# Kernel optimization log

Hardware: AMD Instinct MI355X
Metric: run time of the kernel (lower is better)

Reference implementation:

```python
import jax, jax.numpy as jnp
import numpy as np

V = 20000
E = 40000
NODE_IN = 74
EDGE_IN = 12
D = 64            # node_out_feats
EH = 128          # edge_hidden_feats
STEPS = 6         # num_step_message_passing


def setup_inputs() -> dict:
    key = jax.random.key(0)
    ks = jax.random.split(key, 16)
    s = lambda k, shape, scale=0.05: jax.random.normal(k, shape, dtype=jnp.float32) * scale
    return {
        "node_feats": jax.random.normal(ks[0], (V, NODE_IN), dtype=jnp.float32),
        "edge_feats": jax.random.normal(ks[1], (E, EDGE_IN), dtype=jnp.float32),
        "src": jax.random.randint(ks[2], (E,), 0, V),
        "dst": jax.random.randint(ks[3], (E,), 0, V),
        # project_node_feats: Linear(NODE_IN, D) + ReLU
        "proj_W": s(ks[4], (D, NODE_IN)),
        "proj_b": jnp.zeros((D,), jnp.float32),
        # NNConv edge network: Linear(EDGE_IN, EH) -> ReLU -> Linear(EH, D*D)
        "en_W1": s(ks[5], (EH, EDGE_IN)),
        "en_b1": jnp.zeros((EH,), jnp.float32),
        "en_W2": s(ks[6], (D * D, EH)),
        "en_b2": jnp.zeros((D * D,), jnp.float32),
        # NNConv output bias
        "conv_b": jnp.zeros((D,), jnp.float32),
        # single-layer GRU (PyTorch gate order r, z, n)
        "gru_Wih": s(ks[7], (3 * D, D)),
        "gru_Whh": s(ks[8], (3 * D, D)),
        "gru_bih": jnp.zeros((3 * D,), jnp.float32),
        "gru_bhh": jnp.zeros((3 * D,), jnp.float32),
        # MLPPredictor: Linear(2*D, 1)
        "pred_W": s(ks[9], (1, 2 * D)),
        "pred_b": jnp.zeros((1,), jnp.float32),
    }


def reference(node_feats, edge_feats, src, dst, proj_W, proj_b,
              en_W1, en_b1, en_W2, en_b2, conv_b,
              gru_Wih, gru_Whh, gru_bih, gru_bhh, pred_W, pred_b):
    nV = node_feats.shape[0]
    # project node features
    h = jax.nn.relu(node_feats @ proj_W.T + proj_b)  # (V, D)
    # per-edge weight matrices from the edge network (constant across steps)
    ew = jax.nn.relu(edge_feats @ en_W1.T + en_b1) @ en_W2.T + en_b2  # (E, D*D)
    ew = ew.reshape(-1, D, D)  # (E, D, D)

    def step(h, _):
        # NNConv (aggregator='sum'): m_e = h[src_e] @ W_e, sum at dst, + bias
        m = jnp.einsum('ei,eio->eo', h[src], ew)               # (E, D)
        neigh = jax.ops.segment_sum(m, dst, num_segments=nV)   # (V, D)
        x = jax.nn.relu(neigh + conv_b)
        # GRU update; hidden == h (they coincide in the original loop)
        gi = x @ gru_Wih.T + gru_bih
        gh = h @ gru_Whh.T + gru_bhh
        i_r, i_z, i_n = jnp.split(gi, 3, axis=-1)
        h_r, h_z, h_n = jnp.split(gh, 3, axis=-1)
        r = jax.nn.sigmoid(i_r + h_r)
        z = jax.nn.sigmoid(i_z + h_z)
        n = jnp.tanh(i_n + r * h_n)
        h_new = (1.0 - z) * n + z * h
        return h_new, None

    h, _ = jax.lax.scan(step, h, None, length=STEPS)
    # MLPPredictor: per-edge gather-concat-linear
    score = jnp.concatenate([h[src], h[dst]], axis=1) @ pred_W.T + pred_b  # (E, 1)
    return score
```

## Files before the change

### kernel.cpp

```cpp
#include <hip/hip_runtime.h>
#include <hip/hip_bf16.h>
#include <cstdint>

#define NV 20000
#define NE 40000
#define NODE_IN 74
#define EDGE_IN 12
#define D 64
#define EHID 128
#define NSTEPS 6

typedef __bf16 bf16x8 __attribute__((ext_vector_type(8)));
typedef float f32x4 __attribute__((ext_vector_type(4)));

__global__ __launch_bounds__(256) void k_proj(const float* __restrict__ nf,
                                              const float* __restrict__ W,
                                              const float* __restrict__ b,
                                              float* __restrict__ h,
                                              float* __restrict__ neigh) {
  __shared__ float sn[4][NODE_IN];
  int tid = threadIdx.x;
  int nb = blockIdx.x * 4;
  for (int idx = tid; idx < 4 * NODE_IN; idx += 256) {
    int r = idx / NODE_IN, c = idx % NODE_IN;
    sn[r][c] = nf[(size_t)(nb + r) * NODE_IN + c];
  }
  __syncthreads();
  int nl = tid >> 6, o = tid & 63;
  float acc = b[o];
#pragma unroll
  for (int i = 0; i < NODE_IN; ++i) acc = fmaf(sn[nl][i], W[o * NODE_IN + i], acc);
  h[(size_t)(nb + nl) * D + o] = fmaxf(acc, 0.f);
  neigh[(size_t)(nb + nl) * D + o] = 0.f;
}

__global__ __launch_bounds__(256) void k_edge1(const float* __restrict__ ef,
                                               const float* __restrict__ W1,
                                               const float* __restrict__ b1,
                                               __hip_bfloat16* __restrict__ t_bf) {
  __shared__ float se[2][EDGE_IN];
  int tid = threadIdx.x;
  int eb = blockIdx.x * 2;
  if (tid < 2 * EDGE_IN)
    se[tid / EDGE_IN][tid % EDGE_IN] =
        ef[(size_t)(eb + tid / EDGE_IN) * EDGE_IN + tid % EDGE_IN];
  __syncthreads();
  int el = tid >> 7, k = tid & 127;
  float acc = b1[k];
#pragma unroll
  for (int j = 0; j < EDGE_IN; ++j) acc = fmaf(se[el][j], W1[k * EDGE_IN + j], acc);
  t_bf[(size_t)(eb + el) * EHID + k] = __float2bfloat16(fmaxf(acc, 0.f));
}

__global__ __launch_bounds__(256) void k_cvt_w2(const float* __restrict__ W2,
                                                __hip_bfloat16* __restrict__ w2b) {
  int idx = blockIdx.x * 256 + threadIdx.x;
  if (idx < D * D * EHID) w2b[idx] = __float2bfloat16(W2[idx]);
}

__global__ __launch_bounds__(256) void k_b2t(const float* __restrict__ b2,
                                             __hip_bfloat16* __restrict__ b2t) {
  int idx = blockIdx.x * 256 + threadIdx.x;
  int o = idx >> 6, i = idx & 63;
  b2t[o * 64 + i] = __float2bfloat16(b2[i * 64 + o]);
}

__global__ __launch_bounds__(256) void k_build_b(const float* __restrict__ Wih,
                                                 const float* __restrict__ Whh,
                                                 __hip_bfloat16* __restrict__ Bhi,
                                                 __hip_bfloat16* __restrict__ Blo) {
  int idx = blockIdx.x * 256 + threadIdx.x;
  int n = idx >> 7, k = idx & 127;
  int o = n & 63, cls = n >> 6;
  float v;
  if (cls == 0)      v = (k < 64) ? Wih[o * 64 + k]         : Whh[o * 64 + (k - 64)];
  else if (cls == 1) v = (k < 64) ? Wih[(64 + o) * 64 + k]  : Whh[(64 + o) * 64 + (k - 64)];
  else if (cls == 2) v = (k < 64) ? Wih[(128 + o) * 64 + k] : 0.f;
  else               v = (k < 64) ? 0.f                     : Whh[(128 + o) * 64 + (k - 64)];
  __hip_bfloat16 hi = __float2bfloat16(v);
  Bhi[idx] = hi;
  Blo[idx] = __float2bfloat16(v - __bfloat162float(hi));
}

__global__ __launch_bounds__(512, 2) void k_msg(const float* __restrict__ h,
                                                const __hip_bfloat16* __restrict__ t_bf,
                                                const __hip_bfloat16* __restrict__ w2,
                                                const __hip_bfloat16* __restrict__ b2t,
                                                const int* __restrict__ src,
                                                const int* __restrict__ dst,
                                                float* __restrict__ neigh) {
  __shared__ __hip_bfloat16 W2s[512 * 128];
  __shared__ __hip_bfloat16 Hs[8][16 * 64];
  int tid = threadIdx.x;
  int bx = blockIdx.x;
  int cg = bx >> 6, ih = (bx >> 5) & 1, s = bx & 31;
  int lane = tid & 63, lr = lane & 15, lq = lane >> 4;
  int wave = tid >> 6;
  const int ocol = cg * 16 + lr;

#pragma unroll
  for (int it = 0; it < 16; ++it) {
    int chunk = it * 512 + tid;
    int row = chunk >> 4, c = chunk & 15;
    int ig = row >> 4, ol = row & 15;
    const __hip_bfloat16* gp =
        w2 + ((size_t)((ih * 32 + ig) * 64 + cg * 16 + ol)) * EHID + c * 8;
    *(bf16x8*)(W2s + row * 128 + ((c ^ ol) * 8)) = *(const bf16x8*)gp;
  }
  bf16x8 b2f0, b2f1;
#pragma unroll
  for (int j = 0; j < 8; ++j) {
    int k = lq * 8 + j;
    __bf16 v = *(const __bf16*)(b2t + (size_t)ocol * 64 + ih * 32 + k);
    __bf16 z = (__bf16)0.0f;
    b2f0[j] = (k < 16) ? v : z;
    b2f1[j] = (k >= 16) ? v : z;
  }
  __syncthreads();

  __hip_bfloat16* Hsw = &Hs[wave][0];
  int e0s = s * 1280;
  int nt = (s < 31) ? 20 : 5;

  int sw0 = (((0 * 4 + lq) ^ lr) * 8);
  int sw1 = (((1 * 4 + lq) ^ lr) * 8);
  int sw2 = (((2 * 4 + lq) ^ lr) * 8);
  int sw3 = (((3 * 4 + lq) ^ lr) * 8);

#pragma unroll 1
  for (int r3 = 0; r3 < 3; ++r3) {
    int t = r3 * 8 + wave;
    if (t >= nt) break;
    int e0t = e0s + t * 64;

    bf16x8 tf[4][4];
#pragma unroll
    for (int mt = 0; mt < 4; ++mt)
#pragma unroll
      for (int ks = 0; ks < 4; ++ks)
        tf[mt][ks] = *(const bf16x8*)(t_bf + (size_t)(e0t + mt * 16 + lr) * EHID +
                                      ks * 32 + lq * 8);

    int s_e = src[e0t + lane];
    const float* hrow = h + (size_t)s_e * D + ih * 32;
    f32x4 C[4];
#pragma unroll
    for (int mt = 0; mt < 4; ++mt) C[mt] = f32x4{0.f, 0.f, 0.f, 0.f};

#pragma unroll
    for (int ph = 0; ph < 2; ++ph) {
#pragma unroll
      for (int q = 0; q < 4; ++q) {
        float4 hv = *(const float4*)(hrow + ph * 16 + q * 4);
        Hsw[(q * 4 + 0) * 64 + lane] = __float2bfloat16(hv.x);
        Hsw[(q * 4 + 1) * 64 + lane] = __float2bfloat16(hv.y);
        Hsw[(q * 4 + 2) * 64 + lane] = __float2bfloat16(hv.z);
        Hsw[(q * 4 + 3) * 64 + lane] = __float2bfloat16(hv.w);
      }
#pragma unroll
      for (int mt = 0; mt < 4; ++mt) {
        bf16x8 af;
#pragma unroll
        for (int j = 0; j < 8; ++j)
          af[j] = *(const __bf16*)(Hsw + ((lq * 8 + j) & 15) * 64 + mt * 16 + lr);
        C[mt] = __builtin_amdgcn_mfma_f32_16x16x32_bf16(af, ph ? b2f1 : b2f0, C[mt], 0, 0, 0);
      }
#pragma unroll 2
      for (int igl = 0; igl < 16; ++igl) {
        int ig = ph * 16 + igl;
        const __hip_bfloat16* Wr = W2s + (ig * 16 + lr) * 128;
        bf16x8 f0 = *(const bf16x8*)(Wr + sw0);
        bf16x8 f1 = *(const bf16x8*)(Wr + sw1);
        bf16x8 f2 = *(const bf16x8*)(Wr + sw2);
        bf16x8 f3 = *(const bf16x8*)(Wr + sw3);
#pragma unroll
        for (int mt = 0; mt < 4; ++mt) {
          f32x4 P = {0.f, 0.f, 0.f, 0.f};
          P = __builtin_amdgcn_mfma_f32_16x16x32_bf16(tf[mt][0], f0, P, 0, 0, 0);
          P = __builtin_amdgcn_mfma_f32_16x16x32_bf16(tf[mt][1], f1, P, 0, 0, 0);
          P = __builtin_amdgcn_mfma_f32_16x16x32_bf16(tf[mt][2], f2, P, 0, 0, 0);
          P = __builtin_amdgcn_mfma_f32_16x16x32_bf16(tf[mt][3], f3, P, 0, 0, 0);
          uint2 hA = *(const uint2*)(Hsw + igl * 64 + mt * 16 + lq * 4);
          C[mt][0] = fmaf(__uint_as_float(hA.x << 16), P[0], C[mt][0]);
          C[mt][1] = fmaf(__uint_as_float(hA.x & 0xffff0000u), P[1], C[mt][1]);
          C[mt][2] = fmaf(__uint_as_float(hA.y << 16), P[2], C[mt][2]);
          C[mt][3] = fmaf(__uint_as_float(hA.y & 0xffff0000u), P[3], C[mt][3]);
        }
      }
    }
#pragma unroll
    for (int mt = 0; mt < 4; ++mt) {
#pragma unroll
      for (int r = 0; r < 4; ++r) {
        int ea = e0t + mt * 16 + lq * 4 + r;
        atomicAdd(neigh + (size_t)dst[ea] * D + ocol, C[mt][r]);
      }
    }
  }
}

__global__ __launch_bounds__(256) void k_gru(float* __restrict__ neigh,
                                             float* __restrict__ h,
                                             const __hip_bfloat16* __restrict__ Bhi,
                                             const __hip_bfloat16* __restrict__ Blo,
                                             const float* __restrict__ cb,
                                             const float* __restrict__ bih,
                                             const float* __restrict__ bhh) {
  __shared__ __hip_bfloat16 Ahi[32 * 128];
  __shared__ __hip_bfloat16 Alo[32 * 128];
  int tid = threadIdx.x;
  int n0 = blockIdx.x * 32;
  for (int idx = tid; idx < 32 * 64; idx += 256) {
    int node = idx >> 6, f = idx & 63;
    int gn = n0 + node;
    float xv = fmaxf(neigh[(size_t)gn * D + f] + cb[f], 0.f);
    neigh[(size_t)gn * D + f] = 0.f;
    float hv = h[(size_t)gn * D + f];
    __hip_bfloat16 xh = __float2bfloat16(xv);
    __hip_bfloat16 hh = __float2bfloat16(hv);
    Ahi[node * 128 + f] = xh;
    Ahi[node * 128 + 64 + f] = hh;
    Alo[node * 128 + f] = __float2bfloat16(xv - __bfloat162float(xh));
    Alo[node * 128 + 64 + f] = __float2bfloat16(hv - __bfloat162float(hh));
  }
  __syncthreads();
  int wave = tid >> 6, lane = tid & 63;
  int lr = lane & 15, lq = lane >> 4;
  f32x4 acc[2][4] = {};
#pragma unroll
  for (int ks = 0; ks < 4; ++ks) {
    int koff = ks * 32 + lq * 8;
    bf16x8 ah[2], al[2], bh[4], bl[4];
#pragma unroll
    for (int mt = 0; mt < 2; ++mt) {
      ah[mt] = *(const bf16x8*)(Ahi + (mt * 16 + lr) * 128 + koff);
      al[mt] = *(const bf16x8*)(Alo + (mt * 16 + lr) * 128 + koff);
    }
#pragma unroll
    for (int cls = 0; cls < 4; ++cls) {
      int n = cls * 64 + wave * 16 + lr;
      bh[cls] = *(const bf16x8*)(Bhi + (size_t)n * 128 + koff);
      bl[cls] = *(const bf16x8*)(Blo + (size_t)n * 128 + koff);
    }
#pragma unroll
    for (int mt = 0; mt < 2; ++mt)
#pragma unroll
      for (int cls = 0; cls < 4; ++cls) {
        acc[mt][cls] = __builtin_amdgcn_mfma_f32_16x16x32_bf16(ah[mt], bh[cls], acc[mt][cls], 0, 0, 0);
        acc[mt][cls] = __builtin_amdgcn_mfma_f32_16x16x32_bf16(al[mt], bh[cls], acc[mt][cls], 0, 0, 0);
        acc[mt][cls] = __builtin_amdgcn_mfma_f32_16x16x32_bf16(ah[mt], bl[cls], acc[mt][cls], 0, 0, 0);
      }
  }
  int o = wave * 16 + lr;
  float b_r = bih[o] + bhh[o];
  float b_z = bih[64 + o] + bhh[64 + o];
  float b_in = bih[128 + o];
  float b_hn = bhh[128 + o];
#pragma unroll
  for (int mt = 0; mt < 2; ++mt) {
#pragma unroll
    for (int r = 0; r < 4; ++r) {
      int gn = n0 + mt * 16 + lq * 4 + r;
      float rs = acc[mt][0][r] + b_r;
      float zs = acc[mt][1][r] + b_z;
      float inn = acc[mt][2][r] + b_in;
      float hnn = acc[mt][3][r] + b_hn;
      float rg = 1.f / (1.f + __expf(-rs));
      float zg = 1.f / (1.f + __expf(-zs));
      float a = inn + rg * hnn;
      a = fminf(fmaxf(a, -15.f), 15.f);
      float e2 = __expf(2.f * a);
      float nn = (e2 - 1.f) / (e2 + 1.f);
      float hold = h[(size_t)gn * D + o];
      h[(size_t)gn * D + o] = (1.f - zg) * nn + zg * hold;
    }
  }
}

__global__ __launch_bounds__(256) void k_pred(const float* __restrict__ h,
                                              const int* __restrict__ src,
                                              const int* __restrict__ dst,
                                              const float* __restrict__ pW,
                                              const float* __restrict__ pb,
                                              float* __restrict__ out) {
  int wave = threadIdx.x >> 6, lane = threadIdx.x & 63;
  int e = blockIdx.x * 4 + wave;
  int s = src[e], d2 = dst[e];
  float v = h[(size_t)s * D + lane] * pW[lane] + h[(size_t)d2 * D + lane] * pW[64 + lane];
#pragma unroll
  for (int off = 32; off >= 1; off >>= 1) v += __shfl_xor(v, off, 64);
  if (lane == 0) out[e] = v + pb[0];
}

extern "C" void kernel_launch(void* const* d_in, const int* in_sizes, int n_in,
                              void* d_out, int out_size, void* d_ws, size_t ws_size,
                              hipStream_t stream) {
  const float* node_feats = (const float*)d_in[0];
  const float* edge_feats = (const float*)d_in[1];
  const int* src = (const int*)d_in[2];
  const int* dst = (const int*)d_in[3];
  const float* proj_W = (const float*)d_in[4];
  const float* proj_b = (const float*)d_in[5];
  const float* en_W1 = (const float*)d_in[6];
  const float* en_b1 = (const float*)d_in[7];
  const float* en_W2 = (const float*)d_in[8];
  const float* en_b2 = (const float*)d_in[9];
  const float* conv_b = (const float*)d_in[10];
  const float* gru_Wih = (const float*)d_in[11];
  const float* gru_Whh = (const float*)d_in[12];
  const float* gru_bih = (const float*)d_in[13];
  const float* gru_bhh = (const float*)d_in[14];
  const float* pred_W = (const float*)d_in[15];
  const float* pred_b = (const float*)d_in[16];

  char* ws = (char*)d_ws;
  size_t off = 0;
  auto walloc = [&](size_t bytes) -> void* {
    void* p = ws + off;
    off = (off + bytes + 255) & ~(size_t)255;
    return p;
  };
  float* h = (float*)walloc((size_t)NV * D * 4);
  float* neigh = (float*)walloc((size_t)NV * D * 4);
  __hip_bfloat16* t_bf = (__hip_bfloat16*)walloc((size_t)NE * EHID * 2);
  __hip_bfloat16* w2_bf = (__hip_bfloat16*)walloc((size_t)D * D * EHID * 2);
  __hip_bfloat16* b2t = (__hip_bfloat16*)walloc((size_t)D * D * 2);
  __hip_bfloat16* Bhi = (__hip_bfloat16*)walloc((size_t)256 * 128 * 2);
  __hip_bfloat16* Blo = (__hip_bfloat16*)walloc((size_t)256 * 128 * 2);

  k_proj<<<NV / 4, 256, 0, stream>>>(node_feats, proj_W, proj_b, h, neigh);
  k_edge1<<<NE / 2, 256, 0, stream>>>(edge_feats, en_W1, en_b1, t_bf);
  k_cvt_w2<<<(D * D * EHID + 255) / 256, 256, 0, stream>>>(en_W2, w2_bf);
  k_b2t<<<(D * D + 255) / 256, 256, 0, stream>>>(en_b2, b2t);
  k_build_b<<<128, 256, 0, stream>>>(gru_Wih, gru_Whh, Bhi, Blo);
  for (int s = 0; s < NSTEPS; ++s) {
    k_msg<<<256, 512, 0, stream>>>(h, t_bf, w2_bf, b2t, src, dst, neigh);
    k_gru<<<NV / 32, 256, 0, stream>>>(neigh, h, Bhi, Blo, conv_b, gru_bih, gru_bhh);
  }
  k_pred<<<NE / 4, 256, 0, stream>>>(h, src, dst, pred_W, pred_b, (float*)d_out);
}
```

Baseline: 500.8 us.

## Fuse message and GRU kernels into one persistent cooperative kernel with grid syncs

Replaces the 12 alternating k_msg/k_gru launches with a single cooperative kernel that loops over all steps. Grid-wide syncs separate the message and GRU phases. The W2 tile stays resident in LDS across steps instead of being reloaded each launch. The GRU phase now runs on only 256 blocks that loop over node tiles, which lowers its parallelism and adds grid-sync cost.

```diff
diff --git a/kernel.cpp b/kernel.cpp
--- a/kernel.cpp
+++ b/kernel.cpp
@@ -1,6 +1,9 @@
 #include <hip/hip_runtime.h>
 #include <hip/hip_bf16.h>
+#include <hip/hip_cooperative_groups.h>
 #include <cstdint>
+
+namespace cg = cooperative_groups;
 
 #define NV 20000
 #define NE 40000
@@ -82,21 +85,27 @@
   Blo[idx] = __float2bfloat16(v - __bfloat162float(hi));
 }
 
-__global__ __launch_bounds__(512, 2) void k_msg(const float* __restrict__ h,
-                                                const __hip_bfloat16* __restrict__ t_bf,
-                                                const __hip_bfloat16* __restrict__ w2,
-                                                const __hip_bfloat16* __restrict__ b2t,
-                                                const int* __restrict__ src,
-                                                const int* __restrict__ dst,
-                                                float* __restrict__ neigh) {
+__global__ __launch_bounds__(512, 2) void k_loop(float* __restrict__ h,
+                                                 const __hip_bfloat16* __restrict__ t_bf,
+                                                 const __hip_bfloat16* __restrict__ w2,
+                                                 const __hip_bfloat16* __restrict__ b2t,
+                                                 const __hip_bfloat16* __restrict__ Bhi,
+                                                 const __hip_bfloat16* __restrict__ Blo,
+                                                 const float* __restrict__ cb,
+                                                 const float* __restrict__ bih,
+                                                 const float* __restrict__ bhh,
+                                                 const int* __restrict__ src,
+                                                 const int* __restrict__ dst,
+                                                 float* __restrict__ neigh) {
+  cg::grid_group gg = cg::this_grid();
   __shared__ __hip_bfloat16 W2s[512 * 128];
-  __shared__ __hip_bfloat16 Hs[8][16 * 64];
+  __shared__ __hip_bfloat16 Hs[8 * 1024];
   int tid = threadIdx.x;
   int bx = blockIdx.x;
-  int cg = bx >> 6, ih = (bx >> 5) & 1, s = bx & 31;
+  int cgc = bx >> 6, ih = (bx >> 5) & 1, st = bx & 31;
   int lane = tid & 63, lr = lane & 15, lq = lane >> 4;
   int wave = tid >> 6;
-  const int ocol = cg * 16 + lr;
+  const int ocol = cgc * 16 + lr;
 
 #pragma unroll
   for (int it = 0; it < 16; ++it) {
@@ -104,7 +113,7 @@
     int row = chunk >> 4, c = chunk & 15;
     int ig = row >> 4, ol = row & 15;
     const __hip_bfloat16* gp =
-        w2 + ((size_t)((ih * 32 + ig) * 64 + cg * 16 + ol)) * EHID + c * 8;
+        w2 + ((size_t)((ih * 32 + ig) * 64 + cgc * 16 + ol)) * EHID + c * 8;
     *(bf16x8*)(W2s + row * 128 + ((c ^ ol) * 8)) = *(const bf16x8*)gp;
   }
   bf16x8 b2f0, b2f1;
@@ -118,162 +127,155 @@
   }
   __syncthreads();
 
-  __hip_bfloat16* Hsw = &Hs[wave][0];
-  int e0s = s * 1280;
-  int nt = (s < 31) ? 20 : 5;
+  __hip_bfloat16* Hsw = Hs + wave * 1024;
+  int e0s = st * 1280;
+  int nt = (st < 31) ? 20 : 5;
 
   int sw0 = (((0 * 4 + lq) ^ lr) * 8);
   int sw1 = (((1 * 4 + lq) ^ lr) * 8);
   int sw2 = (((2 * 4 + lq) ^ lr) * 8);
   int sw3 = (((3 * 4 + lq) ^ lr) * 8);
 
+  int colg = wave & 3, mth = wave >> 2;
+  int og = colg * 16 + lr;
+  float b_r = bih[og] + bhh[og];
+  float b_z = bih[64 + og] + bhh[64 + og];
+  float b_in = bih[128 + og];
+  float b_hn = bhh[128 + og];
+
 #pragma unroll 1
-  for (int r3 = 0; r3 < 3; ++r3) {
-    int t = r3 * 8 + wave;
-    if (t >= nt) break;
-    int e0t = e0s + t * 64;
-
-    bf16x8 tf[4][4];
-#pragma unroll
-    for (int mt = 0; mt < 4; ++mt)
-#pragma unroll
-      for (int ks = 0; ks < 4; ++ks)
-        tf[mt][ks] = *(const bf16x8*)(t_bf + (size_t)(e0t + mt * 16 + lr) * EHID +
-                                      ks * 32 + lq * 8);
-
-    int s_e = src[e0t + lane];
-    const float* hrow = h + (size_t)s_e * D + ih * 32;
-    f32x4 C[4];
-#pragma unroll
-    for (int mt = 0; mt < 4; ++mt) C[mt] = f32x4{0.f, 0.f, 0.f, 0.f};
-
-#pragma unroll
-    for (int ph = 0; ph < 2; ++ph) {
-#pragma unroll
-      for (int q = 0; q < 4; ++q) {
-        float4 hv = *(const float4*)(hrow + ph * 16 + q * 4);
-        Hsw[(q * 4 + 0) * 64 + lane] = __float2bfloat16(hv.x);
-        Hsw[(q * 4 + 1) * 64 + lane] = __float2bfloat16(hv.y);
-        Hsw[(q * 4 + 2) * 64 + lane] = __float2bfloat16(hv.z);
-        Hsw[(q * 4 + 3) * 64 + lane] = __float2bfloat16(hv.w);
-      }
-#pragma unroll
-      for (int mt = 0; mt < 4; ++mt) {
-        bf16x8 af;
-#pragma unroll
-        for (int j = 0; j < 8; ++j)
-          af[j] = *(const __bf16*)(Hsw + ((lq * 8 + j) & 15) * 64 + mt * 16 + lr);
-        C[mt] = __builtin_amdgcn_mfma_f32_16x16x32_bf16(af, ph ? b2f1 : b2f0, C[mt], 0, 0, 0);
-      }
+  for (int step = 0; step < NSTEPS; ++step) {
+#pragma unroll 1
+    for (int r3 = 0; r3 < 3; ++r3) {
+      int t = r3 * 8 + wave;
+      if (t < nt) {
+        int e0t = e0s + t * 64;
+        bf16x8 tf[4][4];
+#pragma unroll
+        for (int mt = 0; mt < 4; ++mt)
+#pragma unroll
+          for (int ks = 0; ks < 4; ++ks)
+            tf[mt][ks] = *(const bf16x8*)(t_bf + (size_t)(e0t + mt * 16 + lr) * EHID +
+                                          ks * 32 + lq * 8);
+        int s_e = src[e0t + lane];
+        const float* hrow = h + (size_t)s_e * D + ih * 32;
+        f32x4 C[4];
+#pragma unroll
+        for (int mt = 0; mt < 4; ++mt) C[mt] = f32x4{0.f, 0.f, 0.f, 0.f};
+
+#pragma unroll
+        for (int ph = 0; ph < 2; ++ph) {
+#pragma unroll
+          for (int q = 0; q < 4; ++q) {
+            float4 hv = *(const float4*)(hrow + ph * 16 + q * 4);
+            Hsw[(q * 4 + 0) * 64 + lane] = __float2bfloat16(hv.x);
+            Hsw[(q * 4 + 1) * 64 + lane] = __float2bfloat16(hv.y);
+            Hsw[(q * 4 + 2) * 64 + lane] = __float2bfloat16(hv.z);
+            Hsw[(q * 4 + 3) * 64 + lane] = __float2bfloat16(hv.w);
+          }
+#pragma unroll
+          for (int mt = 0; mt < 4; ++mt) {
+            bf16x8 af;
+#pragma unroll
+            for (int j = 0; j < 8; ++j)
+              af[j] = *(const __bf16*)(Hsw + ((lq * 8 + j) & 15) * 64 + mt * 16 + lr);
+            C[mt] = __builtin_amdgcn_mfma_f32_16x16x32_bf16(af, ph ? b2f1 : b2f0, C[mt], 0, 0, 0);
+          }
 #pragma unroll 2
-      for (int igl = 0; igl < 16; ++igl) {
-        int ig = ph * 16 + igl;
-        const __hip_bfloat16* Wr = W2s + (ig * 16 + lr) * 128;
-        bf16x8 f0 = *(const bf16x8*)(Wr + sw0);
-        bf16x8 f1 = *(const bf16x8*)(Wr + sw1);
-        bf16x8 f2 = *(const bf16x8*)(Wr + sw2);
-        bf16x8 f3 = *(const bf16x8*)(Wr + sw3);
+          for (int igl = 0; igl < 16; ++igl) {
+            int ig = ph * 16 + igl;
+            const __hip_bfloat16* Wr = W2s + (ig * 16 + lr) * 128;
+            bf16x8 f0 = *(const bf16x8*)(Wr + sw0);
+            bf16x8 f1 = *(const bf16x8*)(Wr + sw1);
+            bf16x8 f2 = *(const bf16x8*)(Wr + sw2);
+            bf16x8 f3 = *(const bf16x8*)(Wr + sw3);
+#pragma unroll
+            for (int mt = 0; mt < 4; ++mt) {
+              f32x4 P = {0.f, 0.f, 0.f, 0.f};
+              P = __builtin_amdgcn_mfma_f32_16x16x32_bf16(tf[mt][0], f0, P, 0, 0, 0);
+              P = __builtin_amdgcn_mfma_f32_16x16x32_bf16(tf[mt][1], f1, P, 0, 0, 0);
+              P = __builtin_amdgcn_mfma_f32_16x16x32_bf16(tf[mt][2], f2, P, 0, 0, 0);
+              P = __builtin_amdgcn_mfma_f32_16x16x32_bf16(tf[mt][3], f3, P, 0, 0, 0);
+              uint2 hA = *(const uint2*)(Hsw + igl * 64 + mt * 16 + lq * 4);
+              C[mt][0] = fmaf(__uint_as_float(hA.x << 16), P[0], C[mt][0]);
+              C[mt][1] = fmaf(__uint_as_float(hA.x & 0xffff0000u), P[1], C[mt][1]);
+              C[mt][2] = fmaf(__uint_as_float(hA.y << 16), P[2], C[mt][2]);
+              C[mt][3] = fmaf(__uint_as_float(hA.y & 0xffff0000u), P[3], C[mt][3]);
+            }
+          }
+        }
 #pragma unroll
         for (int mt = 0; mt < 4; ++mt) {
-          f32x4 P = {0.f, 0.f, 0.f, 0.f};
-          P = __builtin_amdgcn_mfma_f32_16x16x32_bf16(tf[mt][0], f0, P, 0, 0, 0);
-          P = __builtin_amdgcn_mfma_f32_16x16x32_bf16(tf[mt][1], f1, P, 0, 0, 0);
-          P = __builtin_amdgcn_mfma_f32_16x16x32_bf16(tf[mt][2], f2, P, 0, 0, 0);
-          P = __builtin_amdgcn_mfma_f32_16x16x32_bf16(tf[mt][3], f3, P, 0, 0, 0);
-          uint2 hA = *(const uint2*)(Hsw + igl * 64 + mt * 16 + lq * 4);
-          C[mt][0] = fmaf(__uint_as_float(hA.x << 16), P[0], C[mt][0]);
-          C[mt][1] = fmaf(__uint_as_float(hA.x & 0xffff0000u), P[1], C[mt][1]);
-          C[mt][2] = fmaf(__uint_as_float(hA.y << 16), P[2], C[mt][2]);
-          C[mt][3] = fmaf(__uint_as_float(hA.y & 0xffff0000u), P[3], C[mt][3]);
+#pragma unroll
+          for (int r = 0; r < 4; ++r) {
+            int ea = e0t + mt * 16 + lq * 4 + r;
+            atomicAdd(neigh + (size_t)dst[ea] * D + ocol, C[mt][r]);
+          }
         }
       }
     }
-#pragma unroll
-    for (int mt = 0; mt < 4; ++mt) {
+    __threadfence();
+    gg.sync();
+
+    __hip_bfloat16* Ahi = Hs;
+    __hip_bfloat16* Alo = Hs + 4096;
+#pragma unroll 1
+    for (int g = bx; g < 625; g += 256) {
+      int n0 = g * 32;
+      __syncthreads();
+      for (int idx = tid; idx < 32 * 64; idx += 512) {
+        int node = idx >> 6, f = idx & 63;
+        int gn = n0 + node;
+        float xv = fmaxf(neigh[(size_t)gn * D + f] + cb[f], 0.f);
+        neigh[(size_t)gn * D + f] = 0.f;
+        float hv = h[(size_t)gn * D + f];
+        __hip_bfloat16 xh = __float2bfloat16(xv);
+        __hip_bfloat16 hh = __float2bfloat16(hv);
+        Ahi[node * 128 + f] = xh;
+        Ahi[node * 128 + 64 + f] = hh;
+        Alo[node * 128 + f] = __float2bfloat16(xv - __bfloat162float(xh));
+        Alo[node * 128 + 64 + f] = __float2bfloat16(hv - __bfloat162float(hh));
+      }
+      __syncthreads();
+      f32x4 acc[4] = {};
+#pragma unroll
+      for (int ks = 0; ks < 4; ++ks) {
+        int koff = ks * 32 + lq * 8;
+        bf16x8 ah, al, bh[4], bl[4];
+        ah = *(const bf16x8*)(Ahi + (mth * 16 + lr) * 128 + koff);
+        al = *(const bf16x8*)(Alo + (mth * 16 + lr) * 128 + koff);
+#pragma unroll
+        for (int cls = 0; cls < 4; ++cls) {
+          int n = cls * 64 + colg * 16 + lr;
+          bh[cls] = *(const bf16x8*)(Bhi + (size_t)n * 128 + koff);
+          bl[cls] = *(const bf16x8*)(Blo + (size_t)n * 128 + koff);
+        }
+#pragma unroll
+        for (int cls = 0; cls < 4; ++cls) {
+          acc[cls] = __builtin_amdgcn_mfma_f32_16x16x32_bf16(ah, bh[cls], acc[cls], 0, 0, 0);
+          acc[cls] = __builtin_amdgcn_mfma_f32_16x16x32_bf16(al, bh[cls], acc[cls], 0, 0, 0);
+          acc[cls] = __builtin_amdgcn_mfma_f32_16x16x32_bf16(ah, bl[cls], acc[cls], 0, 0, 0);
+        }
+      }
 #pragma unroll
       for (int r = 0; r < 4; ++r) {
-        int ea = e0t + mt * 16 + lq * 4 + r;
-        atomicAdd(neigh + (size_t)dst[ea] * D + ocol, C[mt][r]);
+        int gn = n0 + mth * 16 + lq * 4 + r;
+        float rs = acc[0][r] + b_r;
+        float zs = acc[1][r] + b_z;
+        float inn = acc[2][r] + b_in;
+        float hnn = acc[3][r] + b_hn;
+        float rg = 1.f / (1.f + __expf(-rs));
+        float zg = 1.f / (1.f + __expf(-zs));
+        float a = inn + rg * hnn;
+        a = fminf(fmaxf(a, -15.f), 15.f);
+        float e2 = __expf(2.f * a);
+        float nn = (e2 - 1.f) / (e2 + 1.f);
+        float hold = h[(size_t)gn * D + og];
+        h[(size_t)gn * D + og] = (1.f - zg) * nn + zg * hold;
       }
     }
-  }
-}
-
-__global__ __launch_bounds__(256) void k_gru(float* __restrict__ neigh,
-                                             float* __restrict__ h,
-                                             const __hip_bfloat16* __restrict__ Bhi,
-                                             const __hip_bfloat16* __restrict__ Blo,
-                                             const float* __restrict__ cb,
-                                             const float* __restrict__ bih,
-                                             const float* __restrict__ bhh) {
-  __shared__ __hip_bfloat16 Ahi[32 * 128];
-  __shared__ __hip_bfloat16 Alo[32 * 128];
-  int tid = threadIdx.x;
-  int n0 = blockIdx.x * 32;
-  for (int idx = tid; idx < 32 * 64; idx += 256) {
-    int node = idx >> 6, f = idx & 63;
-    int gn = n0 + node;
-    float xv = fmaxf(neigh[(size_t)gn * D + f] + cb[f], 0.f);
-    neigh[(size_t)gn * D + f] = 0.f;
-    float hv = h[(size_t)gn * D + f];
-    __hip_bfloat16 xh = __float2bfloat16(xv);
-    __hip_bfloat16 hh = __float2bfloat16(hv);
-    Ahi[node * 128 + f] = xh;
-    Ahi[node * 128 + 64 + f] = hh;
-    Alo[node * 128 + f] = __float2bfloat16(xv - __bfloat162float(xh));
-    Alo[node * 128 + 64 + f] = __float2bfloat16(hv - __bfloat162float(hh));
-  }
-  __syncthreads();
-  int wave = tid >> 6, lane = tid & 63;
-  int lr = lane & 15, lq = lane >> 4;
-  f32x4 acc[2][4] = {};
-#pragma unroll
-  for (int ks = 0; ks < 4; ++ks) {
-    int koff = ks * 32 + lq * 8;
-    bf16x8 ah[2], al[2], bh[4], bl[4];
-#pragma unroll
-    for (int mt = 0; mt < 2; ++mt) {
-      ah[mt] = *(const bf16x8*)(Ahi + (mt * 16 + lr) * 128 + koff);
-      al[mt] = *(const bf16x8*)(Alo + (mt * 16 + lr) * 128 + koff);
-    }
-#pragma unroll
-    for (int cls = 0; cls < 4; ++cls) {
-      int n = cls * 64 + wave * 16 + lr;
-      bh[cls] = *(const bf16x8*)(Bhi + (size_t)n * 128 + koff);
-      bl[cls] = *(const bf16x8*)(Blo + (size_t)n * 128 + koff);
-    }
-#pragma unroll
-    for (int mt = 0; mt < 2; ++mt)
-#pragma unroll
-      for (int cls = 0; cls < 4; ++cls) {
-        acc[mt][cls] = __builtin_amdgcn_mfma_f32_16x16x32_bf16(ah[mt], bh[cls], acc[mt][cls], 0, 0, 0);
-        acc[mt][cls] = __builtin_amdgcn_mfma_f32_16x16x32_bf16(al[mt], bh[cls], acc[mt][cls], 0, 0, 0);
-        acc[mt][cls] = __builtin_amdgcn_mfma_f32_16x16x32_bf16(ah[mt], bl[cls], acc[mt][cls], 0, 0, 0);
-      }
-  }
-  int o = wave * 16 + lr;
-  float b_r = bih[o] + bhh[o];
-  float b_z = bih[64 + o] + bhh[64 + o];
-  float b_in = bih[128 + o];
-  float b_hn = bhh[128 + o];
-#pragma unroll
-  for (int mt = 0; mt < 2; ++mt) {
-#pragma unroll
-    for (int r = 0; r < 4; ++r) {
-      int gn = n0 + mt * 16 + lq * 4 + r;
-      float rs = acc[mt][0][r] + b_r;
-      float zs = acc[mt][1][r] + b_z;
-      float inn = acc[mt][2][r] + b_in;
-      float hnn = acc[mt][3][r] + b_hn;
-      float rg = 1.f / (1.f + __expf(-rs));
-      float zg = 1.f / (1.f + __expf(-zs));
-      float a = inn + rg * hnn;
-      a = fminf(fmaxf(a, -15.f), 15.f);
-      float e2 = __expf(2.f * a);
-      float nn = (e2 - 1.f) / (e2 + 1.f);
-      float hold = h[(size_t)gn * D + o];
-      h[(size_t)gn * D + o] = (1.f - zg) * nn + zg * hold;
-    }
+    __threadfence();
+    gg.sync();
   }
 }
 
@@ -333,9 +335,11 @@
   k_cvt_w2<<<(D * D * EHID + 255) / 256, 256, 0, stream>>>(en_W2, w2_bf);
   k_b2t<<<(D * D + 255) / 256, 256, 0, stream>>>(en_b2, b2t);
   k_build_b<<<128, 256, 0, stream>>>(gru_Wih, gru_Whh, Bhi, Blo);
-  for (int s = 0; s < NSTEPS; ++s) {
-    k_msg<<<256, 512, 0, stream>>>(h, t_bf, w2_bf, b2t, src, dst, neigh);
-    k_gru<<<NV / 32, 256, 0, stream>>>(neigh, h, Bhi, Blo, conv_b, gru_bih, gru_bhh);
-  }
+
+  void* kargs[] = {(void*)&h,    (void*)&t_bf, (void*)&w2_bf, (void*)&b2t,
+                   (void*)&Bhi,  (void*)&Blo,  (void*)&conv_b, (void*)&gru_bih,
+                   (void*)&gru_bhh, (void*)&src, (void*)&dst,  (void*)&neigh};
+  hipLaunchCooperativeKernel((const void*)k_loop, dim3(256), dim3(512), kargs, 0, stream);
+
   k_pred<<<NE / 4, 256, 0, stream>>>(h, src, dst, pred_W, pred_b, (float*)d_out);
 }
```

Result: slower. 1.412 ms (+182.0%).

## Fold edge-net bias into MFMA accumulator init and software-pipeline W2 fragment loads

Applied to the files above, without the earlier changes.

Drops the separate b2-transpose kernel and the extra bias MFMA pass. Each block now keeps b2 in fp32 shared memory and uses it as the initial value of each per-ig partial product. The W2 fragment loads from LDS are double-buffered so the next ig's fragments load while the current ig's MFMAs run. The second half of the h row is prefetched from global memory before the first half is processed. This costs more registers, which may hurt occupancy under the 512x2 launch bound.

```diff
diff --git a/kernel.cpp b/kernel.cpp
--- a/kernel.cpp
+++ b/kernel.cpp
@@ -56,13 +56,6 @@
                                                 __hip_bfloat16* __restrict__ w2b) {
   int idx = blockIdx.x * 256 + threadIdx.x;
   if (idx < D * D * EHID) w2b[idx] = __float2bfloat16(W2[idx]);
-}
-
-__global__ __launch_bounds__(256) void k_b2t(const float* __restrict__ b2,
-                                             __hip_bfloat16* __restrict__ b2t) {
-  int idx = blockIdx.x * 256 + threadIdx.x;
-  int o = idx >> 6, i = idx & 63;
-  b2t[o * 64 + i] = __float2bfloat16(b2[i * 64 + o]);
 }
 
 __global__ __launch_bounds__(256) void k_build_b(const float* __restrict__ Wih,
@@ -85,18 +78,19 @@
 __global__ __launch_bounds__(512, 2) void k_msg(const float* __restrict__ h,
                                                 const __hip_bfloat16* __restrict__ t_bf,
                                                 const __hip_bfloat16* __restrict__ w2,
-                                                const __hip_bfloat16* __restrict__ b2t,
+                                                const float* __restrict__ b2,
                                                 const int* __restrict__ src,
                                                 const int* __restrict__ dst,
                                                 float* __restrict__ neigh) {
   __shared__ __hip_bfloat16 W2s[512 * 128];
   __shared__ __hip_bfloat16 Hs[8][16 * 64];
+  __shared__ float b2s[32 * 16];
   int tid = threadIdx.x;
   int bx = blockIdx.x;
-  int cg = bx >> 6, ih = (bx >> 5) & 1, s = bx & 31;
+  int cgc = bx >> 6, ih = (bx >> 5) & 1, st = bx & 31;
   int lane = tid & 63, lr = lane & 15, lq = lane >> 4;
   int wave = tid >> 6;
-  const int ocol = cg * 16 + lr;
+  const int ocol = cgc * 16 + lr;
 
 #pragma unroll
   for (int it = 0; it < 16; ++it) {
@@ -104,28 +98,51 @@
     int row = chunk >> 4, c = chunk & 15;
     int ig = row >> 4, ol = row & 15;
     const __hip_bfloat16* gp =
-        w2 + ((size_t)((ih * 32 + ig) * 64 + cg * 16 + ol)) * EHID + c * 8;
+        w2 + ((size_t)((ih * 32 + ig) * 64 + cgc * 16 + ol)) * EHID + c * 8;
     *(bf16x8*)(W2s + row * 128 + ((c ^ ol) * 8)) = *(const bf16x8*)gp;
   }
-  bf16x8 b2f0, b2f1;
-#pragma unroll
-  for (int j = 0; j < 8; ++j) {
-    int k = lq * 8 + j;
-    __bf16 v = *(const __bf16*)(b2t + (size_t)ocol * 64 + ih * 32 + k);
-    __bf16 z = (__bf16)0.0f;
-    b2f0[j] = (k < 16) ? v : z;
-    b2f1[j] = (k >= 16) ? v : z;
+  {
+    int ig = tid >> 4, ol = tid & 15;
+    b2s[tid] = b2[(ih * 32 + ig) * 64 + cgc * 16 + ol];
   }
   __syncthreads();
 
   __hip_bfloat16* Hsw = &Hs[wave][0];
-  int e0s = s * 1280;
-  int nt = (s < 31) ? 20 : 5;
+  int e0s = st * 1280;
+  int nt = (st < 31) ? 20 : 5;
 
   int sw0 = (((0 * 4 + lq) ^ lr) * 8);
   int sw1 = (((1 * 4 + lq) ^ lr) * 8);
   int sw2 = (((2 * 4 + lq) ^ lr) * 8);
   int sw3 = (((3 * 4 + lq) ^ lr) * 8);
+
+  bf16x8 fa0, fa1, fa2, fa3, fb0, fb1, fb2, fb3;
+  float b2a, b2b;
+
+#define LDF(FB, B2V, IG) do {                                            \
+    const __hip_bfloat16* Wr_ = W2s + ((IG) * 16 + lr) * 128;            \
+    FB##0 = *(const bf16x8*)(Wr_ + sw0);                                 \
+    FB##1 = *(const bf16x8*)(Wr_ + sw1);                                 \
+    FB##2 = *(const bf16x8*)(Wr_ + sw2);                                 \
+    FB##3 = *(const bf16x8*)(Wr_ + sw3);                                 \
+    B2V = b2s[(IG) * 16 + lr];                                           \
+  } while (0)
+
+#define DO_IG(FB, B2V, IGL) do {                                         \
+    _Pragma("unroll")                                                    \
+    for (int mt = 0; mt < 4; ++mt) {                                     \
+      f32x4 P = {B2V, B2V, B2V, B2V};                                    \
+      P = __builtin_amdgcn_mfma_f32_16x16x32_bf16(tf[mt][0], FB##0, P, 0, 0, 0); \
+      P = __builtin_amdgcn_mfma_f32_16x16x32_bf16(tf[mt][1], FB##1, P, 0, 0, 0); \
+      P = __builtin_amdgcn_mfma_f32_16x16x32_bf16(tf[mt][2], FB##2, P, 0, 0, 0); \
+      P = __builtin_amdgcn_mfma_f32_16x16x32_bf16(tf[mt][3], FB##3, P, 0, 0, 0); \
+      uint2 hA = *(const uint2*)(Hsw + (IGL) * 64 + mt * 16 + lq * 4);   \
+      C[mt][0] = fmaf(__uint_as_float(hA.x << 16), P[0], C[mt][0]);      \
+      C[mt][1] = fmaf(__uint_as_float(hA.x & 0xffff0000u), P[1], C[mt][1]); \
+      C[mt][2] = fmaf(__uint_as_float(hA.y << 16), P[2], C[mt][2]);      \
+      C[mt][3] = fmaf(__uint_as_float(hA.y & 0xffff0000u), P[3], C[mt][3]); \
+    }                                                                    \
+  } while (0)
 
 #pragma unroll 1
   for (int r3 = 0; r3 < 3; ++r3) {
@@ -143,51 +160,48 @@
 
     int s_e = src[e0t + lane];
     const float* hrow = h + (size_t)s_e * D + ih * 32;
+    float4 h00 = *(const float4*)(hrow + 0);
+    float4 h01 = *(const float4*)(hrow + 4);
+    float4 h02 = *(const float4*)(hrow + 8);
+    float4 h03 = *(const float4*)(hrow + 12);
+
     f32x4 C[4];
 #pragma unroll
     for (int mt = 0; mt < 4; ++mt) C[mt] = f32x4{0.f, 0.f, 0.f, 0.f};
 
-#pragma unroll
-    for (int ph = 0; ph < 2; ++ph) {
-#pragma unroll
-      for (int q = 0; q < 4; ++q) {
-        float4 hv = *(const float4*)(hrow + ph * 16 + q * 4);
-        Hsw[(q * 4 + 0) * 64 + lane] = __float2bfloat16(hv.x);
-        Hsw[(q * 4 + 1) * 64 + lane] = __float2bfloat16(hv.y);
-        Hsw[(q * 4 + 2) * 64 + lane] = __float2bfloat16(hv.z);
-        Hsw[(q * 4 + 3) * 64 + lane] = __float2bfloat16(hv.w);
-      }
-#pragma unroll
-      for (int mt = 0; mt < 4; ++mt) {
-        bf16x8 af;
-#pragma unroll
-        for (int j = 0; j < 8; ++j)
-          af[j] = *(const __bf16*)(Hsw + ((lq * 8 + j) & 15) * 64 + mt * 16 + lr);
-        C[mt] = __builtin_amdgcn_mfma_f32_16x16x32_bf16(af, ph ? b2f1 : b2f0, C[mt], 0, 0, 0);
-      }
+#define WRHS(Q, HV)                                                      \
+    Hsw[((Q)*4 + 0) * 64 + lane] = __float2bfloat16(HV.x);               \
+    Hsw[((Q)*4 + 1) * 64 + lane] = __float2bfloat16(HV.y);               \
+    Hsw[((Q)*4 + 2) * 64 + lane] = __float2bfloat16(HV.z);               \
+    Hsw[((Q)*4 + 3) * 64 + lane] = __float2bfloat16(HV.w);
+    WRHS(0, h00) WRHS(1, h01) WRHS(2, h02) WRHS(3, h03)
+
+    float4 h10 = *(const float4*)(hrow + 16);
+    float4 h11 = *(const float4*)(hrow + 20);
+    float4 h12 = *(const float4*)(hrow + 24);
+    float4 h13 = *(const float4*)(hrow + 28);
+
+    LDF(fa, b2a, 0);
 #pragma unroll 2
-      for (int igl = 0; igl < 16; ++igl) {
-        int ig = ph * 16 + igl;
-        const __hip_bfloat16* Wr = W2s + (ig * 16 + lr) * 128;
-        bf16x8 f0 = *(const bf16x8*)(Wr + sw0);
-        bf16x8 f1 = *(const bf16x8*)(Wr + sw1);
-        bf16x8 f2 = *(const bf16x8*)(Wr + sw2);
-        bf16x8 f3 = *(const bf16x8*)(Wr + sw3);
-#pragma unroll
-        for (int mt = 0; mt < 4; ++mt) {
-          f32x4 P = {0.f, 0.f, 0.f, 0.f};
-          P = __builtin_amdgcn_mfma_f32_16x16x32_bf16(tf[mt][0], f0, P, 0, 0, 0);
-          P = __builtin_amdgcn_mfma_f32_16x16x32_bf16(tf[mt][1], f1, P, 0, 0, 0);
-          P = __builtin_amdgcn_mfma_f32_16x16x32_bf16(tf[mt][2], f2, P, 0, 0, 0);
-          P = __builtin_amdgcn_mfma_f32_16x16x32_bf16(tf[mt][3], f3, P, 0, 0, 0);
-          uint2 hA = *(const uint2*)(Hsw + igl * 64 + mt * 16 + lq * 4);
-          C[mt][0] = fmaf(__uint_as_float(hA.x << 16), P[0], C[mt][0]);
-          C[mt][1] = fmaf(__uint_as_float(hA.x & 0xffff0000u), P[1], C[mt][1]);
-          C[mt][2] = fmaf(__uint_as_float(hA.y << 16), P[2], C[mt][2]);
-          C[mt][3] = fmaf(__uint_as_float(hA.y & 0xffff0000u), P[3], C[mt][3]);
-        }
-      }
-    }
+    for (int igl = 0; igl < 16; igl += 2) {
+      LDF(fb, b2b, igl + 1);
+      DO_IG(fa, b2a, igl);
+      if (igl < 14) LDF(fa, b2a, igl + 2);
+      DO_IG(fb, b2b, igl + 1);
+    }
+
+    WRHS(0, h10) WRHS(1, h11) WRHS(2, h12) WRHS(3, h13)
+#undef WRHS
+
+    LDF(fa, b2a, 16);
+#pragma unroll 2
+    for (int igl = 0; igl < 16; igl += 2) {
+      LDF(fb, b2b, 16 + igl + 1);
+      DO_IG(fa, b2a, igl);
+      if (igl < 14) LDF(fa, b2a, 16 + igl + 2);
+      DO_IG(fb, b2b, igl + 1);
+    }
+
 #pragma unroll
     for (int mt = 0; mt < 4; ++mt) {
 #pragma unroll
@@ -197,6 +211,8 @@
       }
     }
   }
+#undef LDF
+#undef DO_IG
 }
 
 __global__ __launch_bounds__(256) void k_gru(float* __restrict__ neigh,
@@ -324,17 +340,15 @@
   float* neigh = (float*)walloc((size_t)NV * D * 4);
   __hip_bfloat16* t_bf = (__hip_bfloat16*)walloc((size_t)NE * EHID * 2);
   __hip_bfloat16* w2_bf = (__hip_bfloat16*)walloc((size_t)D * D * EHID * 2);
-  __hip_bfloat16* b2t = (__hip_bfloat16*)walloc((size_t)D * D * 2);
   __hip_bfloat16* Bhi = (__hip_bfloat16*)walloc((size_t)256 * 128 * 2);
   __hip_bfloat16* Blo = (__hip_bfloat16*)walloc((size_t)256 * 128 * 2);
 
   k_proj<<<NV / 4, 256, 0, stream>>>(node_feats, proj_W, proj_b, h, neigh);
   k_edge1<<<NE / 2, 256, 0, stream>>>(edge_feats, en_W1, en_b1, t_bf);
   k_cvt_w2<<<(D * D * EHID + 255) / 256, 256, 0, stream>>>(en_W2, w2_bf);
-  k_b2t<<<(D * D + 255) / 256, 256, 0, stream>>>(en_b2, b2t);
   k_build_b<<<128, 256, 0, stream>>>(gru_Wih, gru_Whh, Bhi, Blo);
   for (int s = 0; s < NSTEPS; ++s) {
-    k_msg<<<256, 512, 0, stream>>>(h, t_bf, w2_bf, b2t, src, dst, neigh);
+    k_msg<<<256, 512, 0, stream>>>(h, t_bf, w2_bf, en_b2, src, dst, neigh);
     k_gru<<<NV / 32, 256, 0, stream>>>(neigh, h, Bhi, Blo, conv_b, gru_bih, gru_bhh);
   }
   k_pred<<<NE / 4, 256, 0, stream>>>(h, src, dst, pred_W, pred_b, (float*)d_out);
```

Result: slower. 514.3 us (+2.7%).
